# Performance work log

Hardware: AMD Instinct MI355X
Metric: run time of the kernel (lower is better)

Reference implementation:

```python
import jax, jax.numpy as jnp
import numpy as np

D_MODEL = 1024
NUM_HEADS = 16
D_K = D_MODEL // NUM_HEADS
ROPE_THETA = 10000.0


def apply_rope(x, pos):
    # x: [b, h, t, d], pos: [t] int
    d = x.shape[-1]
    inv_freq = 1.0 / (ROPE_THETA ** (jnp.arange(0, d, 2, dtype=jnp.float32) / d))  # [d/2]
    ang = pos.astype(jnp.float32)[:, None] * inv_freq[None, :]                     # [t, d/2]
    cos = jnp.cos(ang).astype(x.dtype)
    sin = jnp.sin(ang).astype(x.dtype)
    x1 = x[..., 0::2]  # [b,h,t,d/2]
    x2 = x[..., 1::2]
    r1 = x1 * cos - x2 * sin
    r2 = x1 * sin + x2 * cos
    return jnp.stack([r1, r2], axis=-1).reshape(x.shape)


def setup_inputs() -> dict:
    key = jax.random.key(0)
    k1, k2, k3 = jax.random.split(key, 3)
    B, T = 4, 2048
    x = jax.random.normal(k1, (B, T, D_MODEL), dtype=jnp.float32)
    W_qkv = jax.random.normal(k2, (D_MODEL, 3 * D_MODEL), dtype=jnp.float32) * 0.02
    W_o = jax.random.normal(k3, (D_MODEL, D_MODEL), dtype=jnp.float32) * 0.02
    token_positions = jnp.arange(T, dtype=jnp.int32)
    return {"x": x, "W_qkv": W_qkv, "W_o": W_o, "token_positions": token_positions}


def reference(x, W_qkv, W_o, token_positions):
    B, T, _ = x.shape
    H, Dk = NUM_HEADS, D_K
    qkv = x @ W_qkv                                   # [b, t, 3*d_model]
    qkv = qkv.reshape(B, T, 3, H, Dk)                 # last dim ordered (qkv, h, d)
    qkv = jnp.transpose(qkv, (2, 0, 3, 1, 4))         # [3, b, h, t, d]
    q, k, v = qkv[0], qkv[1], qkv[2]
    q = apply_rope(q, token_positions)
    k = apply_rope(k, token_positions)
    scale = 1.0 / jnp.sqrt(jnp.asarray(Dk, dtype=x.dtype))
    scores = jnp.einsum('bhqd,bhkd->bhqk', q, k) * scale
    causal = jnp.tril(jnp.ones((T, T), dtype=bool))
    scores = jnp.where(causal, scores, jnp.asarray(-jnp.inf, dtype=scores.dtype))
    attn = jax.nn.softmax(scores, axis=-1)
    vals = jnp.einsum('bhqk,bhkd->bhqd', attn, v)     # [b, h, t, d]
    out = jnp.transpose(vals, (0, 2, 1, 3)).reshape(B, T, H * Dk)
    return out @ W_o
```

## Files before the change

### kernel.cpp

```cpp
#include <hip/hip_runtime.h>
#include <math.h>

#define B_  4
#define T_  2048
#define DM  1024
#define H_  16
#define DK  64
#define N3  3072

typedef __attribute__((ext_vector_type(8))) __bf16 bf16x8;
typedef __attribute__((ext_vector_type(4))) float f32x4;
typedef __attribute__((ext_vector_type(4))) unsigned int u32x4;

static __device__ __forceinline__ unsigned int f2bf(float f) {
    union { float f; unsigned int u; } v; v.f = f;
    return (v.u + 0x7fffu + ((v.u >> 16) & 1u)) >> 16;
}
static __device__ __forceinline__ unsigned int pack2bf(float a, float b) {
    return f2bf(a) | (f2bf(b) << 16);
}
static __device__ __forceinline__ void gload_lds16(const void* g, void* l) {
    __builtin_amdgcn_global_load_lds(
        (const __attribute__((address_space(1))) unsigned int*)g,
        (__attribute__((address_space(3))) unsigned int*)l, 16, 0, 0);
}

__global__ __launch_bounds__(256)
void convert_copy(const float* __restrict__ src, unsigned short* __restrict__ dst, int n8)
{
    const int i = blockIdx.x * 256 + threadIdx.x;
    if (i >= n8) return;
    const float4 f0 = ((const float4*)src)[i * 2];
    const float4 f1 = ((const float4*)src)[i * 2 + 1];
    u32x4 wv;
    wv.x = pack2bf(f0.x, f0.y); wv.y = pack2bf(f0.z, f0.w);
    wv.z = pack2bf(f1.x, f1.y); wv.w = pack2bf(f1.z, f1.w);
    ((u32x4*)dst)[i] = wv;
}

__global__ __launch_bounds__(256)
void convert_T(const float* __restrict__ src, unsigned short* __restrict__ dst, int K, int N)
{
    __shared__ float tile[32][33];
    const int n0 = blockIdx.x * 32, k0 = blockIdx.y * 32;
    const int tid = threadIdx.x;
    #pragma unroll
    for (int p = 0; p < 4; ++p) {
        const int idx = p * 256 + tid;
        const int r = idx >> 5, c = idx & 31;
        tile[r][c] = src[(size_t)(k0 + r) * N + n0 + c];
    }
    __syncthreads();
    #pragma unroll
    for (int p = 0; p < 4; ++p) {
        const int idx = p * 256 + tid;
        const int r = idx >> 5, c = idx & 31;
        dst[(size_t)(n0 + r) * K + k0 + c] = (unsigned short)f2bf(tile[c][r]);
    }
}

__global__ __launch_bounds__(256)
void rope_table(const int* __restrict__ pos, float2* __restrict__ RC)
{
    const int i = blockIdx.x * 256 + threadIdx.x;
    const int t = i >> 5, dp = i & 31;
    const float ifr = __powf(10000.0f, -(float)(2 * dp) * (1.0f / 64.0f));
    float s, c;
    __sincosf((float)pos[t] * ifr, &s, &c);
    RC[i] = make_float2(c, s);
}

__global__ __launch_bounds__(256, 3)
void qkv_rope_kernel(const unsigned short* __restrict__ xb,
                     const unsigned short* __restrict__ WT,
                     const float2* __restrict__ RC,
                     unsigned short* __restrict__ Qb,
                     unsigned short* __restrict__ Kb,
                     unsigned short* __restrict__ Vtb)
{
    __shared__ u32x4 Asv[3][512];
    __shared__ u32x4 Bsv[3][512];
    const int tid  = threadIdx.x;
    const int lin  = blockIdx.x;
    const int xcd  = lin & 7;
    const int idx  = lin >> 3;
    const int col0 = (xcd * 3 + (idx % 3)) * 128;
    const int row0 = (idx / 3) * 128;
    const int l = tid & 63, w = tid >> 6;
    const int wr = w >> 1, wc = w & 1;
    const int lr = l & 15, hi4 = l >> 4;

    const int srow = tid & 127;
    const int kel  = (tid >> 7) * 8;
    const size_t a0 = (size_t)(row0 + srow) * DM + kel;
    const size_t b0 = (size_t)(col0 + srow) * DM + kel;

    f32x4 acc[4][4];
    #pragma unroll
    for (int m = 0; m < 4; ++m)
        #pragma unroll
        for (int n = 0; n < 4; ++n)
            acc[m][n] = (f32x4){0.f, 0.f, 0.f, 0.f};

    gload_lds16(&xb[a0],      &Asv[0][tid]);
    gload_lds16(&xb[a0 + 16], &Asv[0][256 + tid]);
    gload_lds16(&WT[b0],      &Bsv[0][tid]);
    gload_lds16(&WT[b0 + 16], &Bsv[0][256 + tid]);
    gload_lds16(&xb[a0 + 32], &Asv[1][tid]);
    gload_lds16(&xb[a0 + 48], &Asv[1][256 + tid]);
    gload_lds16(&WT[b0 + 32], &Bsv[1][tid]);
    gload_lds16(&WT[b0 + 48], &Bsv[1][256 + tid]);
    asm volatile("s_waitcnt vmcnt(4)" ::: "memory");
    __builtin_amdgcn_s_barrier();

    #pragma unroll 1
    for (int it = 0; it < 32; ++it) {
        const int cur = it % 3;
        const bool more = (it + 2 < 32);
        if (more) {
            const int nb = (it + 2) % 3;
            const int kn = (it + 2) * 32;
            gload_lds16(&xb[a0 + kn],      &Asv[nb][tid]);
            gload_lds16(&xb[a0 + kn + 16], &Asv[nb][256 + tid]);
            gload_lds16(&WT[b0 + kn],      &Bsv[nb][tid]);
            gload_lds16(&WT[b0 + kn + 16], &Bsv[nb][256 + tid]);
        }
        u32x4 a[4], b[4];
        #pragma unroll
        for (int m = 0; m < 4; ++m) a[m] = Asv[cur][hi4 * 128 + wr * 64 + m * 16 + lr];
        #pragma unroll
        for (int n = 0; n < 4; ++n) b[n] = Bsv[cur][hi4 * 128 + wc * 64 + n * 16 + lr];
        #pragma unroll
        for (int m = 0; m < 4; ++m)
            #pragma unroll
            for (int n = 0; n < 4; ++n)
                acc[m][n] = __builtin_amdgcn_mfma_f32_16x16x32_bf16(
                    __builtin_bit_cast(bf16x8, a[m]),
                    __builtin_bit_cast(bf16x8, b[n]),
                    acc[m][n], 0, 0, 0);
        if (more) asm volatile("s_waitcnt vmcnt(4)" ::: "memory");
        else      asm volatile("s_waitcnt vmcnt(0)" ::: "memory");
        __builtin_amdgcn_s_barrier();
    }

    const int which = col0 >> 10;
    const int h     = ((col0 & 1023) >> 6) + wc;
    const int bb    = row0 >> 11;
    const int t0w   = (row0 & 2047) + wr * 64;

    if (which == 2) {
        #pragma unroll
        for (int n = 0; n < 4; ++n) {
            const int d = n * 16 + lr;
            #pragma unroll
            for (int m = 0; m < 4; ++m) {
                uint2 val;
                val.x = pack2bf(acc[m][n][0], acc[m][n][1]);
                val.y = pack2bf(acc[m][n][2], acc[m][n][3]);
                *(uint2*)&Vtb[((size_t)(bb * H_ + h) * DK + d) * T_ + t0w + m * 16 + hi4 * 4] = val;
            }
        }
    } else {
        unsigned short* dst = (which == 0) ? Qb : Kb;
        const float postscale = (which == 0) ? 0.125f : 1.0f;
        #pragma unroll
        for (int n = 0; n < 4; ++n) {
            const int d  = n * 16 + lr;
            const int dp = d >> 1;
            #pragma unroll
            for (int m = 0; m < 4; ++m)
                #pragma unroll
                for (int r = 0; r < 4; ++r) {
                    const int t = t0w + m * 16 + hi4 * 4 + r;
                    const float v = acc[m][n][r];
                    const float partner = __shfl_xor(v, 1, 64);
                    const float2 cs = RC[t * 32 + dp];
                    const float rv = ((d & 1) ? (partner * cs.y + v * cs.x)
                                              : (v * cs.x - partner * cs.y)) * postscale;
                    dst[((size_t)(bb * H_ + h) * T_ + t) * DK + d] = (unsigned short)f2bf(rv);
                }
        }
    }
}

__global__ __launch_bounds__(512)
void flash_attn_kernel(const unsigned short* __restrict__ Qg,
                       const unsigned short* __restrict__ Kg,
                       const unsigned short* __restrict__ Vtg,
                       unsigned short* __restrict__ Og)
{
    __shared__ u32x4 K4[512];
    __shared__ u32x4 Vt4[512];
    __shared__ unsigned int Pex[8][16 * 36];

    const int tid = threadIdx.x;
    const int l = tid & 63, w = tid >> 6;
    const int lr = l & 15, hi4 = l >> 4;
    const int lin = blockIdx.x;
    const int qt  = 7 - (lin >> 6);
    const int g   = lin & 63;
    const int h   = g & 15, b = g >> 4;
    const int q0 = qt * 256;
    const size_t hb = (size_t)(b * H_ + h) * T_ * DK;
    unsigned int* pw = &Pex[w][0];

    const int srow = tid >> 3, scc = tid & 7;
    const int sdst = srow * 8 + (scc ^ (srow & 7));

    u32x4 qf[2][2];
    #pragma unroll
    for (int m = 0; m < 2; ++m)
        #pragma unroll
        for (int ks = 0; ks < 2; ++ks)
            qf[m][ks] = *(const u32x4*)&Qg[hb + (size_t)(q0 + w * 32 + m * 16 + lr) * DK
                                           + ks * 32 + hi4 * 8];

    f32x4 acc_ot[2][4];
    float m_i[2], l_i[2];
    #pragma unroll
    for (int m = 0; m < 2; ++m) {
        m_i[m] = -INFINITY; l_i[m] = 0.f;
        #pragma unroll
        for (int df = 0; df < 4; ++df) acc_ot[m][df] = (f32x4){0.f, 0.f, 0.f, 0.f};
    }

    const int qwave = q0 + w * 32;
    const int nkt = (q0 >> 6) + 4;

    u32x4 kr = *(const u32x4*)&Kg [hb + (size_t)srow * DK + scc * 8];
    u32x4 vr = *(const u32x4*)&Vtg[hb + (size_t)srow * T_ + scc * 8];

    for (int kt = 0; kt < nkt; ++kt) {
        const int kv0 = kt * 64;
        __syncthreads();
        K4[sdst] = kr; Vt4[sdst] = vr;
        __syncthreads();
        if (kt + 1 < nkt) {
            const int kvn = kv0 + 64;
            kr = *(const u32x4*)&Kg [hb + (size_t)(kvn + srow) * DK + scc * 8];
            vr = *(const u32x4*)&Vtg[hb + (size_t)srow * T_ + kvn + scc * 8];
        }
        if (kv0 > qwave + 31) continue;

        f32x4 st[2][4];
        #pragma unroll
        for (int m = 0; m < 2; ++m)
            #pragma unroll
            for (int nf = 0; nf < 4; ++nf)
                st[m][nf] = (f32x4){0.f, 0.f, 0.f, 0.f};
        #pragma unroll
        for (int ks = 0; ks < 2; ++ks) {
            u32x4 kb4[4];
            #pragma unroll
            for (int nf = 0; nf < 4; ++nf) {
                const int row = nf * 16 + lr;
                kb4[nf] = K4[row * 8 + ((ks * 4 + hi4) ^ (row & 7))];
            }
            #pragma unroll
            for (int m = 0; m < 2; ++m)
                #pragma unroll
                for (int nf = 0; nf < 4; ++nf)
                    st[m][nf] = __builtin_amdgcn_mfma_f32_16x16x32_bf16(
                        __builtin_bit_cast(bf16x8, kb4[nf]),
                        __builtin_bit_cast(bf16x8, qf[m][ks]), st[m][nf], 0, 0, 0);
        }

        const bool needmask = (kv0 + 63 > qwave);
        u32x4 pfrag[2][2];
        #pragma unroll
        for (int m = 0; m < 2; ++m) {
            const int qg = qwave + m * 16 + lr;
            float sv[4][4];
            #pragma unroll
            for (int nf = 0; nf < 4; ++nf)
                #pragma unroll
                for (int r = 0; r < 4; ++r) {
                    float xv = st[m][nf][r];
                    if (needmask && (kv0 + nf * 16 + hi4 * 4 + r) > qg) xv = -INFINITY;
                    sv[nf][r] = xv;
                }
            float mx = sv[0][0];
            #pragma unroll
            for (int nf = 0; nf < 4; ++nf)
                #pragma unroll
                for (int r = 0; r < 4; ++r) mx = fmaxf(mx, sv[nf][r]);
            mx = fmaxf(mx, __shfl_xor(mx, 16, 64));
            mx = fmaxf(mx, __shfl_xor(mx, 32, 64));
            const float mnew = fmaxf(m_i[m], mx);
            const float alpha = __expf(m_i[m] - mnew);
            m_i[m] = mnew;
            float p[4][4], rs = 0.f;
            #pragma unroll
            for (int nf = 0; nf < 4; ++nf)
                #pragma unroll
                for (int r = 0; r < 4; ++r) {
                    p[nf][r] = __expf(sv[nf][r] - mnew);
                    rs += p[nf][r];
                }
            rs += __shfl_xor(rs, 16, 64);
            rs += __shfl_xor(rs, 32, 64);
            l_i[m] = l_i[m] * alpha + rs;
            #pragma unroll
            for (int df = 0; df < 4; ++df) acc_ot[m][df] *= alpha;
            #pragma unroll
            for (int nf = 0; nf < 4; ++nf) {
                uint2 pr;
                pr.x = pack2bf(p[nf][0], p[nf][1]);
                pr.y = pack2bf(p[nf][2], p[nf][3]);
                *(uint2*)&pw[lr * 36 + nf * 8 + hi4 * 2] = pr;
            }
            #pragma unroll
            for (int ks = 0; ks < 2; ++ks)
                pfrag[m][ks] = *(const u32x4*)&pw[lr * 36 + ks * 16 + hi4 * 4];
        }

        #pragma unroll
        for (int ks = 0; ks < 2; ++ks) {
            u32x4 vb[4];
            #pragma unroll
            for (int df = 0; df < 4; ++df) {
                const int d = df * 16 + lr;
                vb[df] = Vt4[d * 8 + ((ks * 4 + hi4) ^ (d & 7))];
            }
            #pragma unroll
            for (int m = 0; m < 2; ++m)
                #pragma unroll
                for (int df = 0; df < 4; ++df)
                    acc_ot[m][df] = __builtin_amdgcn_mfma_f32_16x16x32_bf16(
                        __builtin_bit_cast(bf16x8, vb[df]),
                        __builtin_bit_cast(bf16x8, pfrag[m][ks]), acc_ot[m][df], 0, 0, 0);
        }
    }

    #pragma unroll
    for (int m = 0; m < 2; ++m) {
        const float inv = 1.0f / l_i[m];
        #pragma unroll
        for (int df = 0; df < 4; ++df) {
            uint2 pr;
            pr.x = pack2bf(acc_ot[m][df][0] * inv, acc_ot[m][df][1] * inv);
            pr.y = pack2bf(acc_ot[m][df][2] * inv, acc_ot[m][df][3] * inv);
            *(uint2*)&pw[lr * 36 + df * 8 + hi4 * 2] = pr;
        }
        #pragma unroll
        for (int ks2 = 0; ks2 < 2; ++ks2) {
            const u32x4 ov = *(const u32x4*)&pw[lr * 36 + ks2 * 16 + hi4 * 4];
            *(u32x4*)&Og[hb + (size_t)(qwave + m * 16 + lr) * DK + ks2 * 32 + hi4 * 8] = ov;
        }
    }
}

__global__ __launch_bounds__(256)
void out_proj_kernel(const unsigned short* __restrict__ Ob,
                     const unsigned short* __restrict__ WoT,
                     float* __restrict__ out)
{
    __shared__ u32x4 Asv[512];
    __shared__ u32x4 Bsv[512];
    const int tid  = threadIdx.x;
    const int lin  = blockIdx.x;
    const int col0 = (lin & 7) * 128;
    const int row0 = (lin >> 3) * 128;
    const int l = tid & 63, w = tid >> 6;
    const int wr = w >> 1, wc = w & 1;
    const int lr = l & 15, hi4 = l >> 4;
    const int bb = row0 >> 11, trow0 = row0 & 2047;

    f32x4 acc[4][4];
    #pragma unroll
    for (int m = 0; m < 4; ++m)
        #pragma unroll
        for (int n = 0; n < 4; ++n)
            acc[m][n] = (f32x4){0.f, 0.f, 0.f, 0.f};

    for (int k0 = 0; k0 < DM; k0 += 32) {
        __syncthreads();
        #pragma unroll
        for (int pass = 0; pass < 2; ++pass) {
            const int i = pass * 256 + tid;
            const int row = i & 127, kb = i >> 7;
            const int k = k0 + kb * 8;
            const int hh = k >> 6, dd = k & 63;
            gload_lds16(&Ob[((size_t)(bb * H_ + hh) * T_ + trow0 + row) * DK + dd], &Asv[i]);
            gload_lds16(&WoT[(size_t)(col0 + row) * DM + k0 + kb * 8], &Bsv[i]);
        }
        __syncthreads();
        u32x4 a[4], b[4];
        #pragma unroll
        for (int m = 0; m < 4; ++m) a[m] = Asv[hi4 * 128 + wr * 64 + m * 16 + lr];
        #pragma unroll
        for (int n = 0; n < 4; ++n) b[n] = Bsv[hi4 * 128 + wc * 64 + n * 16 + lr];
        #pragma unroll
        for (int m = 0; m < 4; ++m)
            #pragma unroll
            for (int n = 0; n < 4; ++n)
                acc[m][n] = __builtin_amdgcn_mfma_f32_16x16x32_bf16(
                    __builtin_bit_cast(bf16x8, a[m]),
                    __builtin_bit_cast(bf16x8, b[n]),
                    acc[m][n], 0, 0, 0);
    }

    #pragma unroll
    for (int n = 0; n < 4; ++n) {
        const int gc = col0 + wc * 64 + n * 16 + lr;
        #pragma unroll
        for (int m = 0; m < 4; ++m)
            #pragma unroll
            for (int r = 0; r < 4; ++r)
                out[(size_t)(row0 + wr * 64 + m * 16 + hi4 * 4 + r) * DM + gc] = acc[m][n][r];
    }
}

extern "C" void kernel_launch(void* const* d_in, const int* in_sizes, int n_in,
                              void* d_out, int out_size, void* d_ws, size_t ws_size,
                              hipStream_t stream)
{
    const float* x    = (const float*)d_in[0];
    const float* Wqkv = (const float*)d_in[1];
    const float* Wo   = (const float*)d_in[2];
    const int*   pos  = (const int*)d_in[3];
    float* out = (float*)d_out;

    unsigned short* ws    = (unsigned short*)d_ws;
    unsigned short* xb    = ws;
    unsigned short* WqkvT = xb    + 8388608;
    unsigned short* WoT   = WqkvT + 3145728;
    unsigned short* Qb    = WoT   + 1048576;
    unsigned short* Kb    = Qb    + 8388608;
    unsigned short* Vtb   = Kb    + 8388608;
    unsigned short* Ob    = Vtb   + 8388608;
    float2*         RC    = (float2*)(Ob + 8388608);

    convert_copy<<<dim3(4096), 256, 0, stream>>>(x, xb, 1048576);
    convert_T<<<dim3(96, 32), 256, 0, stream>>>(Wqkv, WqkvT, 1024, 3072);
    convert_T<<<dim3(32, 32), 256, 0, stream>>>(Wo, WoT, 1024, 1024);
    rope_table<<<dim3(256), 256, 0, stream>>>(pos, RC);
    qkv_rope_kernel<<<dim3(1536), 256, 0, stream>>>(xb, WqkvT, RC, Qb, Kb, Vtb);
    flash_attn_kernel<<<dim3(512), 512, 0, stream>>>(Qb, Kb, Vtb, Ob);
    out_proj_kernel<<<dim3(512), 256, 0, stream>>>(Ob, WoT, out);
}
```

Measured before the change: 254.4 us.

## Defer softmax rescale in attention and triple-buffer out-projection loads

The attention inner loop skips the running-max update and the rescale of the accumulator and row sum when every lane's new block max stays within a small margin of the current max. This saves exp and multiply work per tile, in exchange for slightly larger unnormalized exponents. The output projection GEMM moves from a single LDS buffer with two barriers per K-step to a three-stage ring of async global-to-LDS loads issued two steps ahead, using vmcnt waits and one barrier per step. This is meant to overlap load latency with MFMA work, at the cost of triple LDS usage and a launch bound of three blocks per CU.

Measured after the change: 254.7 us. Within noise of the previous version (+0.1%).

```diff
diff --git a/kernel.cpp b/kernel.cpp
--- a/kernel.cpp
+++ b/kernel.cpp
@@ -286,22 +286,26 @@
                 for (int r = 0; r < 4; ++r) mx = fmaxf(mx, sv[nf][r]);
             mx = fmaxf(mx, __shfl_xor(mx, 16, 64));
             mx = fmaxf(mx, __shfl_xor(mx, 32, 64));
-            const float mnew = fmaxf(m_i[m], mx);
-            const float alpha = __expf(m_i[m] - mnew);
-            m_i[m] = mnew;
+            const bool defer = __all((m_i[m] > -1e30f) && (mx <= m_i[m] + 2.0f));
+            if (!defer) {
+                const float mnew = fmaxf(m_i[m], mx);
+                const float alpha = __expf(m_i[m] - mnew);
+                m_i[m] = mnew;
+                l_i[m] *= alpha;
+                #pragma unroll
+                for (int df = 0; df < 4; ++df) acc_ot[m][df] *= alpha;
+            }
             float p[4][4], rs = 0.f;
             #pragma unroll
             for (int nf = 0; nf < 4; ++nf)
                 #pragma unroll
                 for (int r = 0; r < 4; ++r) {
-                    p[nf][r] = __expf(sv[nf][r] - mnew);
+                    p[nf][r] = __expf(sv[nf][r] - m_i[m]);
                     rs += p[nf][r];
                 }
             rs += __shfl_xor(rs, 16, 64);
             rs += __shfl_xor(rs, 32, 64);
-            l_i[m] = l_i[m] * alpha + rs;
-            #pragma unroll
-            for (int df = 0; df < 4; ++df) acc_ot[m][df] *= alpha;
+            l_i[m] += rs;
             #pragma unroll
             for (int nf = 0; nf < 4; ++nf) {
                 uint2 pr;
@@ -350,13 +354,13 @@
     }
 }
 
-__global__ __launch_bounds__(256)
+__global__ __launch_bounds__(256, 3)
 void out_proj_kernel(const unsigned short* __restrict__ Ob,
                      const unsigned short* __restrict__ WoT,
                      float* __restrict__ out)
 {
-    __shared__ u32x4 Asv[512];
-    __shared__ u32x4 Bsv[512];
+    __shared__ u32x4 Asv[3][512];
+    __shared__ u32x4 Bsv[3][512];
     const int tid  = threadIdx.x;
     const int lin  = blockIdx.x;
     const int col0 = (lin & 7) * 128;
@@ -366,6 +370,14 @@
     const int lr = l & 15, hi4 = l >> 4;
     const int bb = row0 >> 11, trow0 = row0 & 2047;
 
+    const int srow = tid & 127;
+    const int kel  = (tid >> 7) * 8;
+    const size_t bsrc = (size_t)(col0 + srow) * DM + kel;
+    auto asrc = [&](int k) -> size_t {
+        const int hh = k >> 6, dd = k & 63;
+        return ((size_t)(bb * H_ + hh) * T_ + trow0 + srow) * DK + dd;
+    };
+
     f32x4 acc[4][4];
     #pragma unroll
     for (int m = 0; m < 4; ++m)
@@ -373,23 +385,34 @@
         for (int n = 0; n < 4; ++n)
             acc[m][n] = (f32x4){0.f, 0.f, 0.f, 0.f};
 
-    for (int k0 = 0; k0 < DM; k0 += 32) {
-        __syncthreads();
-        #pragma unroll
-        for (int pass = 0; pass < 2; ++pass) {
-            const int i = pass * 256 + tid;
-            const int row = i & 127, kb = i >> 7;
-            const int k = k0 + kb * 8;
-            const int hh = k >> 6, dd = k & 63;
-            gload_lds16(&Ob[((size_t)(bb * H_ + hh) * T_ + trow0 + row) * DK + dd], &Asv[i]);
-            gload_lds16(&WoT[(size_t)(col0 + row) * DM + k0 + kb * 8], &Bsv[i]);
-        }
-        __syncthreads();
+    gload_lds16(&Ob[asrc(kel)],           &Asv[0][tid]);
+    gload_lds16(&Ob[asrc(kel + 16)],      &Asv[0][256 + tid]);
+    gload_lds16(&WoT[bsrc],               &Bsv[0][tid]);
+    gload_lds16(&WoT[bsrc + 16],          &Bsv[0][256 + tid]);
+    gload_lds16(&Ob[asrc(32 + kel)],      &Asv[1][tid]);
+    gload_lds16(&Ob[asrc(32 + kel + 16)], &Asv[1][256 + tid]);
+    gload_lds16(&WoT[bsrc + 32],          &Bsv[1][tid]);
+    gload_lds16(&WoT[bsrc + 48],          &Bsv[1][256 + tid]);
+    asm volatile("s_waitcnt vmcnt(4)" ::: "memory");
+    __builtin_amdgcn_s_barrier();
+
+    #pragma unroll 1
+    for (int it = 0; it < 32; ++it) {
+        const int cur = it % 3;
+        const bool more = (it + 2 < 32);
+        if (more) {
+            const int nb = (it + 2) % 3;
+            const int kn = (it + 2) * 32;
+            gload_lds16(&Ob[asrc(kn + kel)],      &Asv[nb][tid]);
+            gload_lds16(&Ob[asrc(kn + kel + 16)], &Asv[nb][256 + tid]);
+            gload_lds16(&WoT[bsrc + kn],          &Bsv[nb][tid]);
+            gload_lds16(&WoT[bsrc + kn + 16],     &Bsv[nb][256 + tid]);
+        }
         u32x4 a[4], b[4];
         #pragma unroll
-        for (int m = 0; m < 4; ++m) a[m] = Asv[hi4 * 128 + wr * 64 + m * 16 + lr];
-        #pragma unroll
-        for (int n = 0; n < 4; ++n) b[n] = Bsv[hi4 * 128 + wc * 64 + n * 16 + lr];
+        for (int m = 0; m < 4; ++m) a[m] = Asv[cur][hi4 * 128 + wr * 64 + m * 16 + lr];
+        #pragma unroll
+        for (int n = 0; n < 4; ++n) b[n] = Bsv[cur][hi4 * 128 + wc * 64 + n * 16 + lr];
         #pragma unroll
         for (int m = 0; m < 4; ++m)
             #pragma unroll
@@ -398,6 +421,9 @@
                     __builtin_bit_cast(bf16x8, a[m]),
                     __builtin_bit_cast(bf16x8, b[n]),
                     acc[m][n], 0, 0, 0);
+        if (more) asm volatile("s_waitcnt vmcnt(4)" ::: "memory");
+        else      asm volatile("s_waitcnt vmcnt(0)" ::: "memory");
+        __builtin_amdgcn_s_barrier();
     }
 
     #pragma unroll
```
